# Kernel tuning notes

Measured on AMD Instinct MI355X. Metric: run time of the kernel, lower is better.

Reference implementation:

```python
import jax, jax.numpy as jnp
import numpy as np

N = 50000   # nodes
E = 400000  # edges
IN = 32     # in_channel
M = 64      # mid_channel
L = 3       # num_layers
EPS = 1e-5


def layer_norm(x, g, b):
    mu = jnp.mean(x, axis=-1, keepdims=True)
    var = jnp.mean((x - mu) ** 2, axis=-1, keepdims=True)
    return (x - mu) / jnp.sqrt(var + EPS) * g + b


def setup_inputs() -> dict:
    key = jax.random.key(0)
    ks = jax.random.split(key, 14)
    s = 0.05
    return {
        "x": jax.random.normal(ks[0], (N, IN), jnp.float32),
        "edge_index": jax.random.randint(ks[1], (2, E), 0, N, jnp.int64),
        # node encoder: Linear(IN->M) + LayerNorm(M)
        "enc_W": jax.random.normal(ks[2], (IN, M), jnp.float32) * s,
        "enc_b": jnp.zeros((M,), jnp.float32),
        "enc_g": jnp.ones((M,), jnp.float32),
        "enc_beta": jnp.zeros((M,), jnp.float32),
        # per-layer pre-norm
        "ln_g": jnp.ones((L, M), jnp.float32),
        "ln_b": jnp.zeros((L, M), jnp.float32),
        # SAGEConvV2 edge MLP: Linear(2M->2M) -> ReLU -> Linear(2M->M)
        "W1": jax.random.normal(ks[3], (L, 2 * M, 2 * M), jnp.float32) * s,
        "b1": jnp.zeros((L, 2 * M), jnp.float32),
        "W2": jax.random.normal(ks[4], (L, 2 * M, M), jnp.float32) * s,
        "b2": jnp.zeros((L, M), jnp.float32),
        # root weight lin_r: Linear(M->M, bias=False)
        "Wr": jax.random.normal(ks[5], (L, M, M), jnp.float32) * s,
    }


def reference(x, edge_index, enc_W, enc_b, enc_g, enc_beta,
              ln_g, ln_b, W1, b1, W2, b2, Wr):
    src = edge_index[0]  # x_j source nodes
    dst = edge_index[1]  # x_i target nodes (aggregation index)
    # node encoder
    x = layer_norm(x @ enc_W + enc_b, enc_g, enc_beta)
    # mean-aggregation denominator (in-degree, clamped to 1 like PyG scatter-mean)
    deg = jax.ops.segment_sum(jnp.ones((E,), x.dtype), dst, num_segments=N)
    deg = jnp.maximum(deg, 1.0)[:, None]
    for l in range(L):  # small fixed layer count
        # res+ block: norm -> act -> (dropout: identity in eval) -> conv -> residual
        h = jax.nn.relu(layer_norm(x, ln_g[l], ln_b[l]))
        # message: concat([x_i, x_j]) -> 2-layer MLP   [E, 2M] -> [E, M]
        msg = jnp.concatenate([h[dst], h[src]], axis=-1)
        msg = jax.nn.relu(msg @ W1[l] + b1[l]) @ W2[l] + b2[l]
        # scatter-mean aggregate at target nodes
        agg = jax.ops.segment_sum(msg, dst, num_segments=N) / deg
        # root weight
        h = agg + h @ Wr[l]
        x = x + h
    return x
```

## Files before the change

### kernel.cpp

```cpp
#include <hip/hip_runtime.h>
#include <hip/hip_bf16.h>

#define N_NODES 50000
#define N_EDGES 400000
#define IN_CH 32
#define EPS 1e-5f
#define SCAN_NB ((N_NODES + 1023) / 1024)
#define EL_CAP 384

#define HIST_B ((N_EDGES + 255) / 256)
#define WCT_TOT (3 * 320 * 64)
#define W2T_TOT (3 * 64 * 128)
#define RPK_B ((WCT_TOT + W2T_TOT + 255) / 256)
#define ENC_B ((N_NODES + 63) / 64)

typedef __attribute__((ext_vector_type(8))) short bh8;
typedef __attribute__((ext_vector_type(4))) float fx4;
typedef __attribute__((ext_vector_type(2))) float fx2;

static __device__ __forceinline__ unsigned int f2bf(float f) {
    __hip_bfloat16 h = __float2bfloat16(f);
    return (unsigned int)*(unsigned short*)&h;
}
static __device__ __forceinline__ unsigned short f2bfu(float f) {
    __hip_bfloat16 h = __float2bfloat16(f);
    return *(unsigned short*)&h;
}
static __device__ __forceinline__ float bflo(unsigned int u) { return __uint_as_float(u << 16); }

__global__ __launch_bounds__(256) void setup_kernel(
    const int* __restrict__ ei, int* __restrict__ cnt,
    const float* __restrict__ W1, const float* __restrict__ Wr,
    const float* __restrict__ W2,
    unsigned short* __restrict__ WcT, unsigned short* __restrict__ W2T,
    const float* __restrict__ x, const float* __restrict__ encW,
    const float* __restrict__ encb, const float* __restrict__ encg,
    const float* __restrict__ encbeta, float* __restrict__ xout) {
    int b = blockIdx.x;
    if (b < HIST_B) {
        int e = b * 256 + threadIdx.x;
        if (e < N_EDGES) atomicAdd(&cnt[ei[N_EDGES + e]], 1);
        return;
    }
    b -= HIST_B;
    if (b < RPK_B) {
        int t = b * 256 + threadIdx.x;
        if (t < WCT_TOT) {
            int l = t / (320 * 64);
            int rem = t % (320 * 64);
            int j = rem / 64, c = rem % 64;
            float v;
            if (j < 128)      v = W1[(l * 128 + c) * 128 + j];
            else if (j < 256) v = W1[(l * 128 + 64 + c) * 128 + (j - 128)];
            else              v = Wr[(l * 64 + c) * 64 + (j - 256)];
            WcT[t] = f2bfu(v);
        } else if (t < WCT_TOT + W2T_TOT) {
            int t2 = t - WCT_TOT;
            int l = t2 / 8192, rem = t2 % 8192;
            int n = rem / 128, k = rem % 128;
            W2T[t2] = f2bfu(W2[l * 8192 + k * 64 + n]);
        }
        return;
    }
    b -= RPK_B;
    __shared__ unsigned short wT[64 * 32];
    int tid = threadIdx.x;
    for (int t = tid; t < IN_CH * 64; t += 256) {
        int k = t >> 6, c = t & 63;
        wT[c * 32 + k] = f2bfu(encW[t]);
    }
    __syncthreads();
    int lane = tid & 63, wid = tid >> 6;
    int l15 = lane & 15, g4 = lane >> 4;
    int node0 = b * 64 + wid * 16;
    int arow = min(node0 + l15, N_NODES - 1);
    float4 xa = *(const float4*)(x + (size_t)arow * 32 + g4 * 8);
    float4 xb = *(const float4*)(x + (size_t)arow * 32 + g4 * 8 + 4);
    bh8 af;
    af[0] = (short)f2bfu(xa.x); af[1] = (short)f2bfu(xa.y);
    af[2] = (short)f2bfu(xa.z); af[3] = (short)f2bfu(xa.w);
    af[4] = (short)f2bfu(xb.x); af[5] = (short)f2bfu(xb.y);
    af[6] = (short)f2bfu(xb.z); af[7] = (short)f2bfu(xb.w);
    float cb[4], gvv[4], bvv[4];
    fx4 cf[4];
    #pragma unroll
    for (int nb = 0; nb < 4; ++nb) {
        int cc = nb * 16 + l15;
        cb[nb] = encb[cc]; gvv[nb] = encg[cc]; bvv[nb] = encbeta[cc];
        bh8 bf = *(const bh8*)&wT[(nb * 16 + l15) * 32 + g4 * 8];
        cf[nb] = __builtin_amdgcn_mfma_f32_16x16x32_bf16(
            af, bf, (fx4){0.f, 0.f, 0.f, 0.f}, 0, 0, 0);
    }
    float vals[4][4];
    #pragma unroll
    for (int nb = 0; nb < 4; ++nb)
        #pragma unroll
        for (int r = 0; r < 4; ++r) vals[nb][r] = cf[nb][r] + cb[nb];
    #pragma unroll
    for (int r = 0; r < 4; ++r) {
        float s = vals[0][r] + vals[1][r] + vals[2][r] + vals[3][r];
        s += __shfl_xor(s, 1, 16);
        s += __shfl_xor(s, 2, 16);
        s += __shfl_xor(s, 4, 16);
        s += __shfl_xor(s, 8, 16);
        float mu = s * (1.f / 64.f);
        float q = 0.f;
        #pragma unroll
        for (int nb = 0; nb < 4; ++nb) { float d = vals[nb][r] - mu; q += d * d; }
        q += __shfl_xor(q, 1, 16);
        q += __shfl_xor(q, 2, 16);
        q += __shfl_xor(q, 4, 16);
        q += __shfl_xor(q, 8, 16);
        float rs = rsqrtf(q * (1.f / 64.f) + EPS);
        int nd = node0 + g4 * 4 + r;
        if (nd < N_NODES) {
            #pragma unroll
            for (int nb = 0; nb < 4; ++nb)
                xout[(size_t)nd * 64 + nb * 16 + l15] =
                    (vals[nb][r] - mu) * rs * gvv[nb] + bvv[nb];
        }
    }
}

__global__ __launch_bounds__(1024) void scan1_kernel(const int* __restrict__ cnt,
                                                     int* __restrict__ exw,
                                                     int* __restrict__ bsum) {
    int b = blockIdx.x, t = threadIdx.x;
    int i = b * 1024 + t;
    int v = (i < N_NODES) ? cnt[i] : 0;
    int lane = t & 63, w = t >> 6;
    int s = v;
    #pragma unroll
    for (int off = 1; off < 64; off <<= 1) {
        int u = __shfl_up(s, off, 64);
        if (lane >= off) s += u;
    }
    __shared__ int ws[16];
    if (lane == 63) ws[w] = s;
    __syncthreads();
    if (t < 16) {
        int sv = ws[t];
        #pragma unroll
        for (int off = 1; off < 16; off <<= 1) {
            int u = __shfl_up(sv, off, 64);
            if (lane >= off) sv += u;
        }
        ws[t] = sv;
    }
    __syncthreads();
    int prefix = (w > 0) ? ws[w - 1] : 0;
    int incl = s + prefix;
    if (i < N_NODES) exw[i] = incl - v;
    if (t == 1023) bsum[b] = incl;
}

__global__ __launch_bounds__(1024) void scan3_kernel(const int* __restrict__ exw,
                                                     const int* __restrict__ bsum,
                                                     int* __restrict__ rp,
                                                     int* __restrict__ cnt) {
    __shared__ int pfx;
    __shared__ int total;
    int b = blockIdx.x, t = threadIdx.x;
    if (t < 64) {
        int v = (t < SCAN_NB) ? bsum[t] : 0;
        #pragma unroll
        for (int off = 1; off < 64; off <<= 1) {
            int u = __shfl_up(v, off, 64);
            if (t >= off) v += u;
        }
        if (b == 0 && t == 0) pfx = 0;
        if (b > 0 && t == b - 1) pfx = v;
        if (t == SCAN_NB - 1) total = v;
    }
    __syncthreads();
    int i = b * 1024 + t;
    if (i < N_NODES) {
        rp[i] = exw[i] + pfx;
        cnt[i] = 0;
    }
    if (b == 0 && t == 0) rp[N_NODES] = total;
}

__global__ void fill_kernel(const int* __restrict__ ei, const int* __restrict__ rp,
                            int* __restrict__ cur, int* __restrict__ el) {
    int e = blockIdx.x * 256 + threadIdx.x;
    if (e < N_EDGES) {
        int d = ei[N_EDGES + e];
        int p = atomicAdd(&cur[d], 1);
        el[rp[d] + p] = ei[e];
    }
}

__global__ __launch_bounds__(256, 8) void fused10_kernel(
    float* __restrict__ x, float* __restrict__ xR,
    const unsigned char* __restrict__ A8I, const unsigned char* __restrict__ B8I,
    const unsigned short* __restrict__ W2T, const float* __restrict__ b2,
    const int* __restrict__ rp, const int* __restrict__ el,
    const float* __restrict__ g, const float* __restrict__ bvec,
    const unsigned short* __restrict__ WcT, const float* __restrict__ b1,
    unsigned char* __restrict__ A8O, unsigned char* __restrict__ B8O, int mode) {
    __shared__ float bufF[1088];
    __shared__ unsigned int slds[16][68];
    __shared__ int el_lds[EL_CAP];
    __shared__ int rp_lds[17];
    float* slds_f = (float*)slds;
    int tid = threadIdx.x;
    int lane = tid & 63, wid = tid >> 6;
    int l15 = lane & 15, g4 = lane >> 4;
    int base = blockIdx.x * 16;
    unsigned int* hU = (unsigned int*)bufF;
    int n = tid >> 4, sq = tid & 15;

    int col = wid * 16 + l15;
    int nd_l = base + g4 * 4;

    if (mode != 0) {
        if (tid < 17) rp_lds[tid] = rp[min(base + tid, N_NODES)];
        __syncthreads();
        int e0 = rp_lds[0];
        int nE = rp_lds[16] - e0;
        bool inl = (nE <= EL_CAP);
        if (inl) for (int t = tid; t < nE; t += 256) el_lds[t] = el[e0 + t];

        int nd_g = base + n;
        float av[8], acc[8];
        {
            uint2 a0 = *(const uint2*)(A8I + (size_t)min(nd_g, N_NODES - 1) * 128 + sq * 8);
            fx2 d0 = __builtin_amdgcn_cvt_pk_f32_fp8((int)a0.x, false);
            fx2 d1 = __builtin_amdgcn_cvt_pk_f32_fp8((int)a0.x, true);
            fx2 d2 = __builtin_amdgcn_cvt_pk_f32_fp8((int)a0.y, false);
            fx2 d3 = __builtin_amdgcn_cvt_pk_f32_fp8((int)a0.y, true);
            av[0] = d0.x; av[1] = d0.y; av[2] = d1.x; av[3] = d1.y;
            av[4] = d2.x; av[5] = d2.y; av[6] = d3.x; av[7] = d3.y;
        }
        #pragma unroll
        for (int i = 0; i < 8; ++i) acc[i] = 0.f;

        float xpre[4];
        #pragma unroll
        for (int r = 0; r < 4; ++r) {
            int nd = min(nd_l + r, N_NODES - 1);
            xpre[r] = xR[(size_t)nd * 64 + col];
        }
        __syncthreads();

        int es = rp_lds[n] - e0, ee = rp_lds[n + 1] - e0;
        int e2 = es;
        int cn = ee - e2; if (cn > 8) cn = 8;
        uint2 bufv[8];
        #pragma unroll
        for (int j = 0; j < 8; ++j)
            if (j < cn) {
                int src = inl ? el_lds[e2 + j] : el[e0 + e2 + j];
                bufv[j] = *(const uint2*)(B8I + (size_t)src * 128 + sq * 8);
            }
        while (cn > 0) {
            #pragma unroll
            for (int j = 0; j < 8; ++j)
                if (j < cn) {
                    fx2 f0 = __builtin_amdgcn_cvt_pk_f32_fp8((int)bufv[j].x, false);
                    fx2 f1 = __builtin_amdgcn_cvt_pk_f32_fp8((int)bufv[j].x, true);
                    fx2 f2 = __builtin_amdgcn_cvt_pk_f32_fp8((int)bufv[j].y, false);
                    fx2 f3 = __builtin_amdgcn_cvt_pk_f32_fp8((int)bufv[j].y, true);
                    acc[0] += fmaxf(av[0] + f0.x, 0.f);
                    acc[1] += fmaxf(av[1] + f0.y, 0.f);
                    acc[2] += fmaxf(av[2] + f1.x, 0.f);
                    acc[3] += fmaxf(av[3] + f1.y, 0.f);
                    acc[4] += fmaxf(av[4] + f2.x, 0.f);
                    acc[5] += fmaxf(av[5] + f2.y, 0.f);
                    acc[6] += fmaxf(av[6] + f3.x, 0.f);
                    acc[7] += fmaxf(av[7] + f3.y, 0.f);
                }
            e2 += cn;
            cn = ee - e2; if (cn > 8) cn = 8;
            #pragma unroll
            for (int j = 0; j < 8; ++j)
                if (j < cn) {
                    int src = inl ? el_lds[e2 + j] : el[e0 + e2 + j];
                    bufv[j] = *(const uint2*)(B8I + (size_t)src * 128 + sq * 8);
                }
        }
        #pragma unroll
        for (int jj = 0; jj < 4; ++jj)
            slds[n][sq * 4 + jj] = f2bf(acc[2 * jj]) | (f2bf(acc[2 * jj + 1]) << 16);
        __syncthreads();

        bh8 sa[4];
        #pragma unroll
        for (int ks = 0; ks < 4; ++ks)
            sa[ks] = *(const bh8*)&slds[l15][ks * 16 + g4 * 4];
        fx4 accm = (fx4){0.f, 0.f, 0.f, 0.f};
        #pragma unroll
        for (int ks = 0; ks < 4; ++ks) {
            bh8 bf = *(const bh8*)(W2T + ((size_t)(wid * 16 + l15) * 128 + ks * 32 + g4 * 8));
            accm = __builtin_amdgcn_mfma_f32_16x16x32_bf16(sa[ks], bf, accm, 0, 0, 0);
        }
        float b2c = b2[col];
        #pragma unroll
        for (int r = 0; r < 4; ++r) {
            int lcl = g4 * 4 + r;
            int cv = rp_lds[lcl + 1] - rp_lds[lcl];
            float inv = cv > 0 ? 1.f / (float)cv : 0.f;
            float msk = cv > 0 ? 1.f : 0.f;
            float xn = xpre[r] + accm[r] * inv + b2c * msk;
            if (mode == 2) x[(size_t)(nd_l + r) * 64 + col] = xn;
            else           bufF[lcl * 68 + col] = xn;
        }
        if (mode == 2) return;
        __syncthreads();
    }

    {
        float vv[4];
        if (mode == 0) {
            int nd = base + n;
            float4 v0 = ((const float4*)(x + (size_t)nd * 64))[sq];
            vv[0] = v0.x; vv[1] = v0.y; vv[2] = v0.z; vv[3] = v0.w;
        } else {
            #pragma unroll
            for (int i = 0; i < 4; ++i) vv[i] = bufF[n * 68 + sq * 4 + i];
        }
        float s = vv[0] + vv[1] + vv[2] + vv[3];
        s += __shfl_xor(s, 1, 16);
        s += __shfl_xor(s, 2, 16);
        s += __shfl_xor(s, 4, 16);
        s += __shfl_xor(s, 8, 16);
        float mu = s * (1.f / 64.f);
        float q = 0.f;
        #pragma unroll
        for (int i = 0; i < 4; ++i) { float d = vv[i] - mu; q += d * d; }
        q += __shfl_xor(q, 1, 16);
        q += __shfl_xor(q, 2, 16);
        q += __shfl_xor(q, 4, 16);
        q += __shfl_xor(q, 8, 16);
        float rs = rsqrtf(q * (1.f / 64.f) + EPS);
        float4 gg = *(const float4*)&g[sq * 4];
        float4 bb = *(const float4*)&bvec[sq * 4];
        float gv[4] = {gg.x, gg.y, gg.z, gg.w};
        float bv[4] = {bb.x, bb.y, bb.z, bb.w};
        __syncthreads();
        #pragma unroll
        for (int i = 0; i < 4; ++i) slds_f[n * 68 + sq * 4 + i] = vv[i];
        #pragma unroll
        for (int jj = 0; jj < 2; ++jj) {
            float h0 = fmaxf((vv[2 * jj] - mu) * rs * gv[2 * jj] + bv[2 * jj], 0.f);
            float h1 = fmaxf((vv[2 * jj + 1] - mu) * rs * gv[2 * jj + 1] + bv[2 * jj + 1], 0.f);
            hU[n * 33 + sq * 2 + jj] = f2bf(h0) | (f2bf(h1) << 16);
        }
    }
    __syncthreads();

    bh8 a2[2];
    #pragma unroll
    for (int ks = 0; ks < 2; ++ks)
        a2[ks] = *(const bh8*)&hU[l15 * 33 + ks * 16 + g4 * 4];
    int ndg = base + g4 * 4;
    #pragma unroll
    for (int nn = 0; nn < 5; ++nn) {
        int nb = wid * 5 + nn;
        fx4 c = (fx4){0.f, 0.f, 0.f, 0.f};
        #pragma unroll
        for (int ks = 0; ks < 2; ++ks) {
            bh8 bf = *(const bh8*)(WcT + ((size_t)(nb * 16 + l15) * 64 + ks * 32 + g4 * 8));
            c = __builtin_amdgcn_mfma_f32_16x16x32_bf16(a2[ks], bf, c, 0, 0, 0);
        }
        int colw = nb * 16 + l15;
        #pragma unroll
        for (int r = 0; r < 4; ++r) {
            int nd = ndg + r;
            float v = c[r];
            if (colw < 128) {
                unsigned int p = __builtin_amdgcn_cvt_pk_fp8_f32(v + b1[colw], 0.f, 0, false);
                A8O[(size_t)nd * 128 + colw] = (unsigned char)(p & 0xFF);
            } else if (colw < 256) {
                unsigned int p = __builtin_amdgcn_cvt_pk_fp8_f32(v, 0.f, 0, false);
                B8O[(size_t)nd * 128 + (colw - 128)] = (unsigned char)(p & 0xFF);
            } else {
                int c2 = colw - 256;
                xR[(size_t)nd * 64 + c2] = slds_f[(g4 * 4 + r) * 68 + c2] + v;
            }
        }
    }
}

extern "C" void kernel_launch(void* const* d_in, const int* in_sizes, int n_in,
                              void* d_out, int out_size, void* d_ws, size_t ws_size,
                              hipStream_t stream) {
    const float* x       = (const float*)d_in[0];
    const int*   ei      = (const int*)d_in[1];
    const float* encW    = (const float*)d_in[2];
    const float* encb    = (const float*)d_in[3];
    const float* encg    = (const float*)d_in[4];
    const float* encbeta = (const float*)d_in[5];
    const float* lng     = (const float*)d_in[6];
    const float* lnb     = (const float*)d_in[7];
    const float* W1      = (const float*)d_in[8];
    const float* b1      = (const float*)d_in[9];
    const float* W2      = (const float*)d_in[10];
    const float* b2      = (const float*)d_in[11];
    const float* Wr      = (const float*)d_in[12];
    float* xout = (float*)d_out;

    char* ws = (char*)d_ws;
    size_t off = 0;
    auto alloc = [&](size_t bytes) -> void* {
        void* p = ws + off;
        off += (bytes + 255) & ~(size_t)255;
        return p;
    };
    unsigned short* WcT  = (unsigned short*)alloc(3 * 320 * 64 * sizeof(unsigned short));
    unsigned short* W2T  = (unsigned short*)alloc(3 * 64 * 128 * sizeof(unsigned short));
    unsigned char*  A80  = (unsigned char*)alloc((size_t)N_NODES * 128);
    unsigned char*  A81  = (unsigned char*)alloc((size_t)N_NODES * 128);
    unsigned char*  B80  = (unsigned char*)alloc((size_t)N_NODES * 128);
    unsigned char*  B81  = (unsigned char*)alloc((size_t)N_NODES * 128);
    float*          xR   = (float*)alloc((size_t)N_NODES * 64 * sizeof(float));
    int*            cnt  = (int*)alloc(N_NODES * sizeof(int));
    int*            rp   = (int*)alloc((N_NODES + 1) * sizeof(int));
    int*            el   = (int*)alloc(N_EDGES * sizeof(int));
    int*            exw  = (int*)alloc(N_NODES * sizeof(int));
    int*            bsum = (int*)alloc(SCAN_NB * sizeof(int));

    hipMemsetAsync(cnt, 0, N_NODES * sizeof(int), stream);
    setup_kernel<<<HIST_B + RPK_B + ENC_B, 256, 0, stream>>>(
        ei, cnt, W1, Wr, W2, WcT, W2T, x, encW, encb, encg, encbeta, xout);
    scan1_kernel<<<SCAN_NB, 1024, 0, stream>>>(cnt, exw, bsum);
    scan3_kernel<<<SCAN_NB, 1024, 0, stream>>>(exw, bsum, rp, cnt);
    fill_kernel<<<(N_EDGES + 255) / 256, 256, 0, stream>>>(ei, rp, cnt, el);

    int gblocks = (N_NODES + 15) / 16;
    fused10_kernel<<<gblocks, 256, 0, stream>>>(
        xout, xR, A80, B80, W2T, b2, rp, el, lng, lnb,
        WcT, b1, A80, B80, 0);
    fused10_kernel<<<gblocks, 256, 0, stream>>>(
        xout, xR, A80, B80, W2T, b2, rp, el, lng + 64, lnb + 64,
        WcT + (size_t)1 * 320 * 64, b1 + 128, A81, B81, 1);
    fused10_kernel<<<gblocks, 256, 0, stream>>>(
        xout, xR, A81, B81, W2T + (size_t)1 * 64 * 128, b2 + 64, rp, el, lng + 128, lnb + 128,
        WcT + (size_t)2 * 320 * 64, b1 + 256, A80, B80, 1);
    fused10_kernel<<<gblocks, 256, 0, stream>>>(
        xout, xR, A80, B80, W2T + (size_t)2 * 64 * 128, b2 + 128, rp, el, lng, lnb,
        WcT, b1, A81, B81, 2);
}
```

Measured before the change: 194.9 us.

## Fuse encoder with layer-0 pre-norm and node projection, drop mode-0 launch

The encoder block now also applies the layer-0 LayerNorm+ReLU and runs the 64x320 node projection with MFMA. It writes the fp8 A/B halves and the residual-plus-root term directly, so the separate mode-0 fused kernel launch and its round trip of x through global memory go away. Weight repacking moves into its own small kernel, launched first so setup can read WcT. Bounds clamps were removed from the fused kernel, which relies on N being a multiple of 16 (50000 is). Setup now depends on the repack kernel finishing, and the encoder blocks do more work.

Result: no change. 196.0 us (+0.6%).

```diff
diff --git a/kernel.cpp b/kernel.cpp
--- a/kernel.cpp
+++ b/kernel.cpp
@@ -11,8 +11,7 @@
 #define HIST_B ((N_EDGES + 255) / 256)
 #define WCT_TOT (3 * 320 * 64)
 #define W2T_TOT (3 * 64 * 128)
-#define RPK_B ((WCT_TOT + W2T_TOT + 255) / 256)
-#define ENC_B ((N_NODES + 63) / 64)
+#define ENC64_B ((N_NODES + 63) / 64)
 
 typedef __attribute__((ext_vector_type(8))) short bh8;
 typedef __attribute__((ext_vector_type(4))) float fx4;
@@ -28,14 +27,37 @@
 }
 static __device__ __forceinline__ float bflo(unsigned int u) { return __uint_as_float(u << 16); }
 
-__global__ __launch_bounds__(256) void setup_kernel(
+__global__ void repack_kernel(const float* __restrict__ W1, const float* __restrict__ Wr,
+                              const float* __restrict__ W2,
+                              unsigned short* __restrict__ WcT,
+                              unsigned short* __restrict__ W2T) {
+    int t = blockIdx.x * 256 + threadIdx.x;
+    if (t < WCT_TOT) {
+        int l = t / (320 * 64);
+        int rem = t % (320 * 64);
+        int j = rem / 64, c = rem % 64;
+        float v;
+        if (j < 128)      v = W1[(l * 128 + c) * 128 + j];
+        else if (j < 256) v = W1[(l * 128 + 64 + c) * 128 + (j - 128)];
+        else              v = Wr[(l * 64 + c) * 64 + (j - 256)];
+        WcT[t] = f2bfu(v);
+    } else if (t < WCT_TOT + W2T_TOT) {
+        int t2 = t - WCT_TOT;
+        int l = t2 / 8192, rem = t2 % 8192;
+        int n = rem / 128, k = rem % 128;
+        W2T[t2] = f2bfu(W2[l * 8192 + k * 64 + n]);
+    }
+}
+
+__global__ __launch_bounds__(256) void setup2_kernel(
     const int* __restrict__ ei, int* __restrict__ cnt,
-    const float* __restrict__ W1, const float* __restrict__ Wr,
-    const float* __restrict__ W2,
-    unsigned short* __restrict__ WcT, unsigned short* __restrict__ W2T,
     const float* __restrict__ x, const float* __restrict__ encW,
     const float* __restrict__ encb, const float* __restrict__ encg,
-    const float* __restrict__ encbeta, float* __restrict__ xout) {
+    const float* __restrict__ encbeta,
+    const float* __restrict__ lng0, const float* __restrict__ lnb0,
+    const unsigned short* __restrict__ WcT0, const float* __restrict__ b1_0,
+    unsigned char* __restrict__ A8O, unsigned char* __restrict__ B8O,
+    float* __restrict__ xR) {
     int b = blockIdx.x;
     if (b < HIST_B) {
         int e = b * 256 + threadIdx.x;
@@ -43,27 +65,8 @@
         return;
     }
     b -= HIST_B;
-    if (b < RPK_B) {
-        int t = b * 256 + threadIdx.x;
-        if (t < WCT_TOT) {
-            int l = t / (320 * 64);
-            int rem = t % (320 * 64);
-            int j = rem / 64, c = rem % 64;
-            float v;
-            if (j < 128)      v = W1[(l * 128 + c) * 128 + j];
-            else if (j < 256) v = W1[(l * 128 + 64 + c) * 128 + (j - 128)];
-            else              v = Wr[(l * 64 + c) * 64 + (j - 256)];
-            WcT[t] = f2bfu(v);
-        } else if (t < WCT_TOT + W2T_TOT) {
-            int t2 = t - WCT_TOT;
-            int l = t2 / 8192, rem = t2 % 8192;
-            int n = rem / 128, k = rem % 128;
-            W2T[t2] = f2bfu(W2[l * 8192 + k * 64 + n]);
-        }
-        return;
-    }
-    b -= RPK_B;
     __shared__ unsigned short wT[64 * 32];
+    __shared__ __attribute__((aligned(16))) unsigned short hS[4][16][72];
     int tid = threadIdx.x;
     for (int t = tid; t < IN_CH * 64; t += 256) {
         int k = t >> 6, c = t & 63;
@@ -81,21 +84,19 @@
     af[2] = (short)f2bfu(xa.z); af[3] = (short)f2bfu(xa.w);
     af[4] = (short)f2bfu(xb.x); af[5] = (short)f2bfu(xb.y);
     af[6] = (short)f2bfu(xb.z); af[7] = (short)f2bfu(xb.w);
-    float cb[4], gvv[4], bvv[4];
-    fx4 cf[4];
+    float cb[4], gvv[4], bvv[4], lg[4], lb[4];
+    float vals[4][4];
     #pragma unroll
     for (int nb = 0; nb < 4; ++nb) {
         int cc = nb * 16 + l15;
         cb[nb] = encb[cc]; gvv[nb] = encg[cc]; bvv[nb] = encbeta[cc];
+        lg[nb] = lng0[cc]; lb[nb] = lnb0[cc];
         bh8 bf = *(const bh8*)&wT[(nb * 16 + l15) * 32 + g4 * 8];
-        cf[nb] = __builtin_amdgcn_mfma_f32_16x16x32_bf16(
+        fx4 cf = __builtin_amdgcn_mfma_f32_16x16x32_bf16(
             af, bf, (fx4){0.f, 0.f, 0.f, 0.f}, 0, 0, 0);
-    }
-    float vals[4][4];
-    #pragma unroll
-    for (int nb = 0; nb < 4; ++nb)
-        #pragma unroll
-        for (int r = 0; r < 4; ++r) vals[nb][r] = cf[nb][r] + cb[nb];
+        #pragma unroll
+        for (int r = 0; r < 4; ++r) vals[nb][r] = cf[r] + cb[nb];
+    }
     #pragma unroll
     for (int r = 0; r < 4; ++r) {
         float s = vals[0][r] + vals[1][r] + vals[2][r] + vals[3][r];
@@ -112,12 +113,60 @@
         q += __shfl_xor(q, 4, 16);
         q += __shfl_xor(q, 8, 16);
         float rs = rsqrtf(q * (1.f / 64.f) + EPS);
-        int nd = node0 + g4 * 4 + r;
-        if (nd < N_NODES) {
-            #pragma unroll
-            for (int nb = 0; nb < 4; ++nb)
-                xout[(size_t)nd * 64 + nb * 16 + l15] =
-                    (vals[nb][r] - mu) * rs * gvv[nb] + bvv[nb];
+        #pragma unroll
+        for (int nb = 0; nb < 4; ++nb)
+            vals[nb][r] = (vals[nb][r] - mu) * rs * gvv[nb] + bvv[nb];
+    }
+    #pragma unroll
+    for (int r = 0; r < 4; ++r) {
+        float s = vals[0][r] + vals[1][r] + vals[2][r] + vals[3][r];
+        s += __shfl_xor(s, 1, 16);
+        s += __shfl_xor(s, 2, 16);
+        s += __shfl_xor(s, 4, 16);
+        s += __shfl_xor(s, 8, 16);
+        float mu = s * (1.f / 64.f);
+        float q = 0.f;
+        #pragma unroll
+        for (int nb = 0; nb < 4; ++nb) { float d = vals[nb][r] - mu; q += d * d; }
+        q += __shfl_xor(q, 1, 16);
+        q += __shfl_xor(q, 2, 16);
+        q += __shfl_xor(q, 4, 16);
+        q += __shfl_xor(q, 8, 16);
+        float rs = rsqrtf(q * (1.f / 64.f) + EPS);
+        #pragma unroll
+        for (int nb = 0; nb < 4; ++nb) {
+            float h = fmaxf((vals[nb][r] - mu) * rs * lg[nb] + lb[nb], 0.f);
+            hS[wid][g4 * 4 + r][nb * 16 + l15] = f2bfu(h);
+        }
+    }
+    __syncthreads();
+    bh8 a2[2];
+    #pragma unroll
+    for (int ks = 0; ks < 2; ++ks)
+        a2[ks] = *(const bh8*)&hS[wid][l15][ks * 32 + g4 * 8];
+    #pragma unroll
+    for (int nb2 = 0; nb2 < 20; ++nb2) {
+        fx4 c = (fx4){0.f, 0.f, 0.f, 0.f};
+        #pragma unroll
+        for (int ks = 0; ks < 2; ++ks) {
+            bh8 bf = *(const bh8*)(WcT0 + ((size_t)(nb2 * 16 + l15) * 64 + ks * 32 + g4 * 8));
+            c = __builtin_amdgcn_mfma_f32_16x16x32_bf16(a2[ks], bf, c, 0, 0, 0);
+        }
+        int colw = nb2 * 16 + l15;
+        #pragma unroll
+        for (int r = 0; r < 4; ++r) {
+            int nd = node0 + g4 * 4 + r;
+            if (nd >= N_NODES) continue;
+            float v = c[r];
+            if (colw < 128) {
+                unsigned int p = __builtin_amdgcn_cvt_pk_fp8_f32(v + b1_0[colw], 0.f, 0, false);
+                A8O[(size_t)nd * 128 + colw] = (unsigned char)(p & 0xFF);
+            } else if (colw < 256) {
+                unsigned int p = __builtin_amdgcn_cvt_pk_fp8_f32(v, 0.f, 0, false);
+                B8O[(size_t)nd * 128 + (colw - 128)] = (unsigned char)(p & 0xFF);
+            } else {
+                xR[(size_t)nd * 64 + (colw - 256)] = vals[nb2 - 16][r] + v;
+            }
         }
     }
 }
@@ -191,7 +240,7 @@
     }
 }
 
-__global__ __launch_bounds__(256, 8) void fused10_kernel(
+__global__ __launch_bounds__(256, 8) void fused15_kernel(
     float* __restrict__ x, float* __restrict__ xR,
     const unsigned char* __restrict__ A8I, const unsigned char* __restrict__ B8I,
     const unsigned short* __restrict__ W2T, const float* __restrict__ b2,
@@ -210,12 +259,11 @@
     int base = blockIdx.x * 16;
     unsigned int* hU = (unsigned int*)bufF;
     int n = tid >> 4, sq = tid & 15;
-
     int col = wid * 16 + l15;
     int nd_l = base + g4 * 4;
 
-    if (mode != 0) {
-        if (tid < 17) rp_lds[tid] = rp[min(base + tid, N_NODES)];
+    {
+        if (tid < 17) rp_lds[tid] = rp[base + tid];
         __syncthreads();
         int e0 = rp_lds[0];
         int nE = rp_lds[16] - e0;
@@ -225,7 +273,7 @@
         int nd_g = base + n;
         float av[8], acc[8];
         {
-            uint2 a0 = *(const uint2*)(A8I + (size_t)min(nd_g, N_NODES - 1) * 128 + sq * 8);
+            uint2 a0 = *(const uint2*)(A8I + (size_t)nd_g * 128 + sq * 8);
             fx2 d0 = __builtin_amdgcn_cvt_pk_f32_fp8((int)a0.x, false);
             fx2 d1 = __builtin_amdgcn_cvt_pk_f32_fp8((int)a0.x, true);
             fx2 d2 = __builtin_amdgcn_cvt_pk_f32_fp8((int)a0.y, false);
@@ -238,10 +286,8 @@
 
         float xpre[4];
         #pragma unroll
-        for (int r = 0; r < 4; ++r) {
-            int nd = min(nd_l + r, N_NODES - 1);
-            xpre[r] = xR[(size_t)nd * 64 + col];
-        }
+        for (int r = 0; r < 4; ++r)
+            xpre[r] = xR[(size_t)(nd_l + r) * 64 + col];
         __syncthreads();
 
         int es = rp_lds[n] - e0, ee = rp_lds[n + 1] - e0;
@@ -312,14 +358,8 @@
 
     {
         float vv[4];
-        if (mode == 0) {
-            int nd = base + n;
-            float4 v0 = ((const float4*)(x + (size_t)nd * 64))[sq];
-            vv[0] = v0.x; vv[1] = v0.y; vv[2] = v0.z; vv[3] = v0.w;
-        } else {
-            #pragma unroll
-            for (int i = 0; i < 4; ++i) vv[i] = bufF[n * 68 + sq * 4 + i];
-        }
+        #pragma unroll
+        for (int i = 0; i < 4; ++i) vv[i] = bufF[n * 68 + sq * 4 + i];
         float s = vv[0] + vv[1] + vv[2] + vv[3];
         s += __shfl_xor(s, 1, 16);
         s += __shfl_xor(s, 2, 16);
@@ -422,23 +462,22 @@
     int*            bsum = (int*)alloc(SCAN_NB * sizeof(int));
 
     hipMemsetAsync(cnt, 0, N_NODES * sizeof(int), stream);
-    setup_kernel<<<HIST_B + RPK_B + ENC_B, 256, 0, stream>>>(
-        ei, cnt, W1, Wr, W2, WcT, W2T, x, encW, encb, encg, encbeta, xout);
+    repack_kernel<<<(WCT_TOT + W2T_TOT + 255) / 256, 256, 0, stream>>>(W1, Wr, W2, WcT, W2T);
+    setup2_kernel<<<HIST_B + ENC64_B, 256, 0, stream>>>(
+        ei, cnt, x, encW, encb, encg, encbeta, lng, lnb,
+        WcT, b1, A80, B80, xR);
     scan1_kernel<<<SCAN_NB, 1024, 0, stream>>>(cnt, exw, bsum);
     scan3_kernel<<<SCAN_NB, 1024, 0, stream>>>(exw, bsum, rp, cnt);
     fill_kernel<<<(N_EDGES + 255) / 256, 256, 0, stream>>>(ei, rp, cnt, el);
 
     int gblocks = (N_NODES + 15) / 16;
-    fused10_kernel<<<gblocks, 256, 0, stream>>>(
-        xout, xR, A80, B80, W2T, b2, rp, el, lng, lnb,
-        WcT, b1, A80, B80, 0);
-    fused10_kernel<<<gblocks, 256, 0, stream>>>(
+    fused15_kernel<<<gblocks, 256, 0, stream>>>(
         xout, xR, A80, B80, W2T, b2, rp, el, lng + 64, lnb + 64,
         WcT + (size_t)1 * 320 * 64, b1 + 128, A81, B81, 1);
-    fused10_kernel<<<gblocks, 256, 0, stream>>>(
+    fused15_kernel<<<gblocks, 256, 0, stream>>>(
         xout, xR, A81, B81, W2T + (size_t)1 * 64 * 128, b2 + 64, rp, el, lng + 128, lnb + 128,
         WcT + (size_t)2 * 320 * 64, b1 + 256, A80, B80, 1);
-    fused10_kernel<<<gblocks, 256, 0, stream>>>(
+    fused15_kernel<<<gblocks, 256, 0, stream>>>(
         xout, xR, A80, B80, W2T + (size_t)2 * 64 * 128, b2 + 128, rp, el, lng, lnb,
         WcT, b1, A81, B81, 2);
 }
```
